# Kernel tuning notes

Hardware: AMD Instinct MI355X
Metric: run time of the kernel (lower is better)

The kernel has to match this reference:

```python
import jax, jax.numpy as jnp
import numpy as np

N = 20000      # nodes
E = 320000     # edges
H = 256        # hidden_dim
BD = 64        # bond embedding dim
MSG_IN = 2 * H + BD  # 576


def setup_inputs() -> dict:
    key = jax.random.key(0)
    ks = jax.random.split(key, 24)
    s = 0.05
    inp = {}
    inp["x"] = jax.random.randint(ks[0], (N, 3), 0, 7).astype(jnp.float32)
    inp["edge_index"] = jax.random.randint(ks[1], (2, E), 0, N).astype(jnp.int32)
    inp["edge_attr"] = jax.random.randint(ks[2], (E, 1), 0, 5).astype(jnp.float32)
    inp["batch"] = jnp.zeros((N,), jnp.int32)
    # embedding tables
    inp["atom_table"] = jax.random.normal(ks[3], (11, 64), jnp.float32) * s
    inp["charge_table"] = jax.random.normal(ks[4], (7, 32), jnp.float32) * s
    inp["hybrid_table"] = jax.random.normal(ks[5], (8, 32), jnp.float32) * s
    inp["bond_table"] = jax.random.normal(ks[6], (5, BD), jnp.float32) * s
    # 3 stacked ChemicalGraphConv layers (weights stored [in, out])
    inp["gnn_w1"] = jax.random.normal(ks[7], (3, MSG_IN, H), jnp.float32) * s
    inp["gnn_b1"] = jnp.zeros((3, H), jnp.float32)
    inp["gnn_w2"] = jax.random.normal(ks[8], (3, H, H), jnp.float32) * s
    inp["gnn_b2"] = jnp.zeros((3, H), jnp.float32)
    inp["att_w"] = jax.random.normal(ks[9], (3, BD, 1), jnp.float32) * s
    inp["att_b"] = jnp.zeros((3, 1), jnp.float32)
    # chemical_properties MLP
    inp["prop_w1"] = jax.random.normal(ks[10], (H, 128), jnp.float32) * s
    inp["prop_b1"] = jnp.zeros((128,), jnp.float32)
    inp["prop_w2"] = jax.random.normal(ks[11], (128, 32), jnp.float32) * s
    inp["prop_b2"] = jnp.zeros((32,), jnp.float32)
    # 4 functional-group pattern encoders, stacked [4, H, 16]
    inp["fg_w"] = jax.random.normal(ks[12], (4, H, 16), jnp.float32) * s
    inp["fg_b"] = jnp.zeros((4, 16), jnp.float32)
    return inp


def reference(x, edge_index, edge_attr, batch,
              atom_table, charge_table, hybrid_table, bond_table,
              gnn_w1, gnn_b1, gnn_w2, gnn_b2, att_w, att_b,
              prop_w1, prop_b1, prop_w2, prop_b2, fg_w, fg_b):
    n = x.shape[0]
    atom_types = jnp.clip(x[:, 0].astype(jnp.int32), 0, 10)
    formal_charges = jnp.clip(x[:, 2].astype(jnp.int32) + 3, 0, 6)
    hybridization = jnp.clip(x[:, 1].astype(jnp.int32), 0, 7)
    bond_types = jnp.clip(edge_attr[:, 0].astype(jnp.int32), 0, 4)
    bond_emb = bond_table[bond_types]  # [E, 64]

    h = jnp.concatenate([atom_table[atom_types],
                         charge_table[formal_charges],
                         hybrid_table[hybridization]], axis=-1)  # [N, 128]
    h = jnp.pad(h, ((0, 0), (0, H - h.shape[1])))  # pad to hidden_dim

    row, col = edge_index[0], edge_index[1]
    for l in range(3):  # 3 ChemicalGraphConv layers
        gate = jax.nn.sigmoid(bond_emb @ att_w[l] + att_b[l])            # [E, 1]
        msg = jnp.concatenate([h[row], h[col], bond_emb], axis=-1)      # [E, 576]
        msg = jax.nn.relu(msg @ gnn_w1[l] + gnn_b1[l]) @ gnn_w2[l] + gnn_b2[l]
        msg = msg * gate                                                 # [E, H]
        h = h + jax.ops.segment_sum(msg, row, num_segments=n)

    chemical_props = jax.nn.relu(h @ prop_w1 + prop_b1) @ prop_w2 + prop_b2  # [N, 32]

    # FunctionalGroupDetector: mean(encoder(h)) == mean(h) @ W + b (linear)
    pooled = jnp.mean(h, axis=0)                                   # [H]
    fg = (jnp.einsum('d,kdo->ko', pooled, fg_w) + fg_b).reshape(-1)  # [64]
    fg_features = jnp.broadcast_to(fg, (n, 64))

    return h, chemical_props, fg_features, atom_types
```

## Files before the change

kernel.cpp:

```cpp
#include <hip/hip_runtime.h>
#include <stdint.h>

typedef unsigned short u16;
typedef unsigned int   u32;
typedef __attribute__((ext_vector_type(8))) short bf16x8;
typedef __attribute__((ext_vector_type(4))) float f32x4;

#define NN 20000
#define NE 320000
#define HD 256
#define BD 64

#define WS_PRE   0u
#define WS_W1T   20480000u
#define WS_W2I   21266432u
#define WS_PW1   21659648u
#define WS_PREB  21725184u
#define WS_GATE  21740544u
#define WS_POOL  21740608u
#define WS_FGV   21741632u
#define WS_CNT   21741888u
#define WS_META  21821888u

__device__ __forceinline__ u16 f2bf(float f){
  u32 u = __float_as_uint(f);
  u += 0x7fffu + ((u >> 16) & 1u);
  return (u16)(u >> 16);
}
__device__ __forceinline__ u32 pk2(float a, float b){
  return (u32)f2bf(a) | ((u32)f2bf(b) << 16);
}
__device__ __forceinline__ float bf2f(u16 u){
  return __uint_as_float((u32)u << 16);
}
__device__ __forceinline__ u32 pk2t(float a, float b){
  return __builtin_amdgcn_perm(__float_as_uint(a), __float_as_uint(b), 0x03020706u);
}
__device__ __forceinline__ u32 relu_pack(u32 a, u32 b, float p0, float p1){
  float a0 = __uint_as_float(a << 16);
  float a1 = __uint_as_float(a & 0xffff0000u);
  float b0 = __uint_as_float(b << 16);
  float b1 = __uint_as_float(b & 0xffff0000u);
  float s0 = fmaxf(a0 + b0 + p0, 0.f);
  float s1 = fmaxf(a1 + b1 + p1, 0.f);
  return pk2t(s0, s1);
}
__device__ __forceinline__ void gl_lds16(const u16* g, u16* l){
  __builtin_amdgcn_global_load_lds(
      (const __attribute__((address_space(1))) unsigned int*)g,
      (__attribute__((address_space(3))) unsigned int*)l, 16, 0, 0);
}

__global__ void setup_k(const float* __restrict__ gw1,
                        const float* __restrict__ gw2,
                        const float* __restrict__ pw1,
                        const float* __restrict__ bond_table,
                        const float* __restrict__ gb1,
                        const float* __restrict__ att_w,
                        const float* __restrict__ att_b,
                        const float* __restrict__ x,
                        const float* __restrict__ atom_table,
                        const float* __restrict__ charge_table,
                        const float* __restrict__ hybrid_table,
                        u16* __restrict__ w1t, u16* __restrict__ w2img,
                        u16* __restrict__ pw1bf, float* __restrict__ preb,
                        float* __restrict__ gate_tab, float* __restrict__ pooled,
                        int* __restrict__ cnt,
                        float* __restrict__ h0, float* __restrict__ out_at){
  int i = blockIdx.x*256 + threadIdx.x;
  if (i < 393216){
    int l = i >> 17;
    int r = i & 131071;
    int c = r >> 8;
    int k = r & 255;
    int srow = (c < 256) ? k : (256 + k);
    w1t[i] = f2bf(gw1[(l*576 + srow)*256 + (c & 255)]);
  } else if (i < 589824){
    int t = i - 393216;
    int j  = t & 7;
    int s  = (t >> 3) & 3;
    int c  = (t >> 5) & 255;
    int ks = (t >> 13) & 7;
    int l  = t >> 16;
    int kc = s ^ ((c >> 1) & 3);
    int k  = ks*32 + kc*8 + j;
    w2img[t] = f2bf(gw2[(l*256 + k)*256 + c]);
  } else if (i < 622592){
    int t = i - 589824;
    int o = t >> 8, k = t & 255;
    pw1bf[t] = f2bf(pw1[k*128 + o]);
  } else if (i < 626432){
    int t = i - 622592;
    int l = t / 1280;
    int r = t - l*1280;
    int bt = r >> 8, c = r & 255;
    float s = gb1[l*HD + c];
    for (int d = 0; d < BD; ++d)
      s += bond_table[bt*BD + d] * gw1[(l*576 + 512 + d)*256 + c];
    preb[(l*5 + bt)*256 + c] = s;
  } else if (i < 626447){
    int t = i - 626432;
    int l = t / 5, b = t - 5*l;
    float s = att_b[l];
    for (int d = 0; d < BD; ++d) s += bond_table[b*BD + d] * att_w[l*BD + d];
    gate_tab[t] = 1.0f / (1.0f + __expf(-s));
  } else if (i < 626703){
    pooled[i - 626447] = 0.0f;
  } else if (i < 646703){
    cnt[i - 626703] = 0;
  } else if (i < 1286703){
    int t = i - 646703;
    int n = t >> 5, sub = t & 31, c0 = sub*8;
    int at = (int)x[n*3 + 0]; at = at < 0 ? 0 : (at > 10 ? 10 : at);
    float4 v0 = {0.f,0.f,0.f,0.f}, v1 = {0.f,0.f,0.f,0.f};
    if (c0 < 64){
      v0 = *(const float4*)(atom_table + at*64 + c0);
      v1 = *(const float4*)(atom_table + at*64 + c0 + 4);
    } else if (c0 < 96){
      int fc = (int)x[n*3 + 2] + 3; fc = fc < 0 ? 0 : (fc > 6 ? 6 : fc);
      v0 = *(const float4*)(charge_table + fc*32 + (c0 - 64));
      v1 = *(const float4*)(charge_table + fc*32 + (c0 - 64) + 4);
    } else if (c0 < 128){
      int hy = (int)x[n*3 + 1]; hy = hy < 0 ? 0 : (hy > 7 ? 7 : hy);
      v0 = *(const float4*)(hybrid_table + hy*32 + (c0 - 96));
      v1 = *(const float4*)(hybrid_table + hy*32 + (c0 - 96) + 4);
    }
    *(float4*)(h0 + (size_t)n*HD + c0)     = v0;
    *(float4*)(h0 + (size_t)n*HD + c0 + 4) = v1;
    if (sub == 0) out_at[n] = (float)at;
  }
}

__global__ void hist_k(const int* __restrict__ eidx, int* __restrict__ cnt){
  int e = blockIdx.x*256 + threadIdx.x;
  int r = eidx[e]; r = r < 0 ? 0 : (r >= NN ? NN-1 : r);
  atomicAdd(&cnt[r], 1);
}

__launch_bounds__(1024)
__global__ void scan_k(int* __restrict__ cnt){
  __shared__ int part[1024];
  int t = threadIdx.x;
  int base = t*20;
  int loc[20];
  int s = 0;
  #pragma unroll
  for (int j = 0; j < 20; ++j){
    int idx = base + j;
    int v = (idx < NN) ? cnt[idx] : 0;
    loc[j] = v; s += v;
  }
  part[t] = s; __syncthreads();
  for (int off = 1; off < 1024; off <<= 1){
    int v = (t >= off) ? part[t-off] : 0;
    __syncthreads();
    part[t] += v;
    __syncthreads();
  }
  int run = part[t] - s;
  #pragma unroll
  for (int j = 0; j < 20; ++j){
    int idx = base + j;
    if (idx < NN){ cnt[idx] = run; run += loc[j]; }
  }
}

__global__ void scatter_k(const int* __restrict__ eidx,
                          const float* __restrict__ eattr,
                          int* __restrict__ cur,
                          int2* __restrict__ smeta){
  int e = blockIdx.x*256 + threadIdx.x;
  int r = eidx[e];        r = r < 0 ? 0 : (r >= NN ? NN-1 : r);
  int c = eidx[NE + e];   c = c < 0 ? 0 : (c >= NN ? NN-1 : c);
  int bt = (int)eattr[e]; bt = bt < 0 ? 0 : (bt > 4 ? 4 : bt);
  int pos = atomicAdd(&cur[r], 1);
  if (pos >= 0 && pos < NE){
    int2 m; m.x = r | (bt << 20); m.y = c;
    smeta[pos] = m;
  }
}

__launch_bounds__(256, 4)
__global__ void pre_k(const float* __restrict__ h,
                      const u16* __restrict__ w1t,
                      u16* __restrict__ pre, int layer){
  __shared__ u16 a_lds[64*40];
  __shared__ u16 b_lds[256*40];
  const int tid = threadIdx.x;
  const int n0 = blockIdx.x * 64;
  const int half = blockIdx.y;
  const int w = tid >> 6, lane = tid & 63, g = lane >> 4, lr = lane & 15;
  const int rstage = tid >> 2, q = tid & 3;
  int arow = n0 + rstage; if (arow >= NN) arow = NN-1;
  const float* hrow = h + (size_t)arow*HD;
  const u16* bp = w1t + ((size_t)layer*512 + (size_t)half*256 + tid)*256;

  f32x4 acc[4][4];
  for (int mi = 0; mi < 4; ++mi)
    for (int nj = 0; nj < 4; ++nj)
      acc[mi][nj] = (f32x4){0.f,0.f,0.f,0.f};

  for (int ks = 0; ks < 8; ++ks){
    __syncthreads();
    {
      const float* src = hrow + ks*32 + q*8;
      float4 f0 = *(const float4*)src;
      float4 f1 = *(const float4*)(src + 4);
      uint4 av;
      av.x = pk2(f0.x,f0.y); av.y = pk2(f0.z,f0.w);
      av.z = pk2(f1.x,f1.y); av.w = pk2(f1.z,f1.w);
      *(uint4*)(a_lds + rstage*40 + q*8) = av;
    }
    {
      const u16* src = bp + ks*32;
      uint4 s0 = *(const uint4*)(src);
      uint4 s1 = *(const uint4*)(src + 8);
      uint4 s2 = *(const uint4*)(src + 16);
      uint4 s3 = *(const uint4*)(src + 24);
      u16* dst = b_lds + tid*40;
      *(uint4*)(dst)      = s0;
      *(uint4*)(dst + 8)  = s1;
      *(uint4*)(dst + 16) = s2;
      *(uint4*)(dst + 24) = s3;
    }
    __syncthreads();
    bf16x8 af[4], bfr[4];
    for (int mi = 0; mi < 4; ++mi)
      af[mi] = *(const bf16x8*)(a_lds + (mi*16 + lr)*40 + g*8);
    for (int nj = 0; nj < 4; ++nj)
      bfr[nj] = *(const bf16x8*)(b_lds + (w*64 + nj*16 + lr)*40 + g*8);
    for (int mi = 0; mi < 4; ++mi)
      for (int nj = 0; nj < 4; ++nj)
        acc[mi][nj] = __builtin_amdgcn_mfma_f32_16x16x32_bf16(af[mi], bfr[nj], acc[mi][nj], 0, 0, 0);
  }

  for (int mi = 0; mi < 4; ++mi)
    for (int nj = 0; nj < 4; ++nj)
      for (int p = 0; p < 4; ++p){
        int re = mi*16 + g*4 + p;
        int n = n0 + re;
        if (n < NN)
          pre[(size_t)n*512 + half*256 + w*64 + nj*16 + lr] = f2bf(acc[mi][nj][p]);
      }
}

__launch_bounds__(512, 4)
__global__ void edge_msg_k(const int2* __restrict__ smeta,
                           const u16* __restrict__ pre,
                           const float* __restrict__ prebg,
                           const u16* __restrict__ w2img,
                           const float* __restrict__ b2g,
                           const float* __restrict__ gate_tab,
                           float* __restrict__ h,
                           int layer){
  __shared__ u16 b_lds[16384];
  __shared__ u16 t_lds[64*264];
  __shared__ int   row_l[64];
  __shared__ float gate_l[64];

  const int tid = threadIdx.x;
  const int bid = blockIdx.x;
  const int blk = (bid & 7)*625 + (bid >> 3);
  const int eBase = blk * 64;
  const int w = tid >> 6, lane = tid & 63, g = lane >> 4, lr = lane & 15;
  const int rstage = tid >> 3, q = tid & 7;

  const size_t wbase = (size_t)layer*65536;

  #pragma unroll
  for (int b = 0; b < 2; ++b)
    #pragma unroll
    for (int j = 0; j < 2; ++j)
      gl_lds16(w2img + wbase + (size_t)(b*256 + w*32 + j*16)*32 + lane*8,
               b_lds + b*8192 + w*1024 + j*512);

  int2 m0 = smeta[eBase + rstage];
  const int rI  = m0.x & 0xFFFFF;
  const int btI = (m0.x >> 20) & 7;
  const int cI  = m0.y;

  if (tid < 64){
    int2 mm = smeta[eBase + tid];
    row_l[tid]  = mm.x & 0xFFFFF;
    gate_l[tid] = gate_tab[layer*5 + ((mm.x >> 20) & 7)];
  }

  {
    const u16* p1 = pre + (size_t)rI*512;
    const u16* p2 = pre + (size_t)cI*512 + 256;
    const float* pb = prebg + (size_t)(layer*5 + btI)*256;
    #pragma unroll
    for (int it = 0; it < 4; ++it){
      int c0 = it*64 + q*8;
      uint4 v1 = *(const uint4*)(p1 + c0);
      uint4 v2 = *(const uint4*)(p2 + c0);
      float4 pa = *(const float4*)(pb + c0);
      float4 pc = *(const float4*)(pb + c0 + 4);
      uint4 ov;
      ov.x = relu_pack(v1.x, v2.x, pa.x, pa.y);
      ov.y = relu_pack(v1.y, v2.y, pa.z, pa.w);
      ov.z = relu_pack(v1.z, v2.z, pc.x, pc.y);
      ov.w = relu_pack(v1.w, v2.w, pc.z, pc.w);
      *(uint4*)(t_lds + rstage*264 + c0) = ov;
    }
  }

  __syncthreads();

  f32x4 acc[4][2];
  for (int mi = 0; mi < 4; ++mi)
    for (int nj = 0; nj < 2; ++nj)
      acc[mi][nj] = (f32x4){0.f,0.f,0.f,0.f};

  const int sw = (g ^ ((lr >> 1) & 3)) << 3;

  #pragma unroll
  for (int ks = 0; ks < 8; ++ks){
    if (ks >= 1 && ks < 7){
      #pragma unroll
      for (int j = 0; j < 2; ++j)
        gl_lds16(w2img + wbase + (size_t)((ks+1)*256 + w*32 + j*16)*32 + lane*8,
                 b_lds + ((ks+1)&1)*8192 + w*1024 + j*512);
      asm volatile("s_waitcnt vmcnt(2)" ::: "memory");
    } else if (ks == 0){
      asm volatile("s_waitcnt vmcnt(2)" ::: "memory");
    } else {
      asm volatile("s_waitcnt vmcnt(0)" ::: "memory");
    }
    const u16* bb = b_lds + (ks&1)*8192 + w*1024;
    bf16x8 af[4], bfr[2];
    for (int nj = 0; nj < 2; ++nj)
      bfr[nj] = *(const bf16x8*)(bb + (nj*16 + lr)*32 + sw);
    for (int mi = 0; mi < 4; ++mi)
      af[mi] = *(const bf16x8*)(t_lds + (mi*16 + lr)*264 + ks*32 + g*8);
    __builtin_amdgcn_s_setprio(1);
    for (int mi = 0; mi < 4; ++mi)
      for (int nj = 0; nj < 2; ++nj)
        acc[mi][nj] = __builtin_amdgcn_mfma_f32_16x16x32_bf16(af[mi], bfr[nj], acc[mi][nj], 0, 0, 0);
    __builtin_amdgcn_s_setprio(0);
  }

  {
    float b2v[2];
    for (int nj = 0; nj < 2; ++nj) b2v[nj] = b2g[layer*HD + w*32 + nj*16 + lr];
    for (int mi = 0; mi < 4; ++mi)
      for (int nj = 0; nj < 2; ++nj){
        u16* mb = b_lds + nj*8192 + w*1024 + lr*64;
        float v[4];
        #pragma unroll
        for (int p = 0; p < 4; ++p){
          int re = mi*16 + g*4 + p;
          v[p] = (acc[mi][nj][p] + b2v[nj]) * gate_l[re];
        }
        int slot = (mi*2 + (g >> 1)) ^ (lr & 7);
        uint2 pkv; pkv.x = pk2t(v[0], v[1]); pkv.y = pk2t(v[2], v[3]);
        *(uint2*)(mb + slot*8 + (g & 1)*4) = pkv;
      }
  }
  __syncthreads();

  {
    const int cl = tid & 255, half = tid >> 8;
    const u16* mb = b_lds + ((cl >> 4) & 1)*8192 + (cl >> 5)*1024 + (cl & 15)*64;
    float run = 0.f;
    int currow = row_l[half*32];
    for (int e8 = half*4; e8 < half*4 + 4; ++e8){
      bf16x8 mv = *(const bf16x8*)(mb + ((e8 ^ (cl & 7)) << 3));
      #pragma unroll
      for (int j = 0; j < 8; ++j){
        int r = row_l[e8*8 + j];
        if (r != currow){
          atomicAdd(h + (size_t)currow*HD + cl, run);
          run = 0.f; currow = r;
        }
        run += bf2f((u16)mv[j]);
      }
    }
    atomicAdd(h + (size_t)currow*HD + cl, run);
  }
}

__global__ void pool_k(const float* __restrict__ h,
                       float* __restrict__ pooled){
  int c = threadIdx.x;
  int r0 = blockIdx.x * 50;
  float s = 0.f;
  for (int r = r0; r < r0 + 50; ++r)
    s += h[(size_t)r*HD + c];
  atomicAdd(&pooled[c], s);
}

__global__ void bcast_fg_k(const float* __restrict__ pooled,
                           const float* __restrict__ fg_w,
                           const float* __restrict__ fg_b,
                           float* __restrict__ out_fg){
  __shared__ float fv[64];
  int tid = threadIdx.x;
  if (tid < 64){
    int k = tid >> 4, j = tid & 15;
    float s = 0.f;
    for (int d = 0; d < HD; ++d) s += pooled[d] * fg_w[(size_t)k*HD*16 + d*16 + j];
    fv[tid] = s / (float)NN + fg_b[k*16 + j];
  }
  __syncthreads();
  int i = blockIdx.x*256 + tid;
  out_fg[i] = fv[i & 63];
}

__launch_bounds__(256, 3)
__global__ void props_mfma_k(const float* __restrict__ h,
                             const u16* __restrict__ pw1bf,
                             const float* __restrict__ pb1,
                             const float* __restrict__ pw2,
                             const float* __restrict__ pb2,
                             float* __restrict__ outp){
  __shared__ u16 a_lds[64*40];
  __shared__ u16 b2_lds[128*40];
  __shared__ u16 t2[64*136];
  __shared__ float w2s[128*32];
  const int tid = threadIdx.x;
  const int n0 = blockIdx.x*64;
  const int w = tid >> 6, lane = tid & 63, g = lane >> 4, lr = lane & 15;
  const int rstage = tid >> 2, q = tid & 3;
  int arow = n0 + rstage; if (arow >= NN) arow = NN-1;
  const float* hrow = h + (size_t)arow*HD;

  for (int j = 0; j < 4; ++j)
    *(float4*)(w2s + tid*16 + j*4) = *(const float4*)(pw2 + tid*16 + j*4);

  const int colb = tid >> 1, halfb = tid & 1;

  f32x4 acc[4][2];
  for (int mi = 0; mi < 4; ++mi)
    for (int nj = 0; nj < 2; ++nj)
      acc[mi][nj] = (f32x4){0.f,0.f,0.f,0.f};

  for (int ks = 0; ks < 8; ++ks){
    __syncthreads();
    {
      const float* src = hrow + ks*32 + q*8;
      float4 f0 = *(const float4*)src;
      float4 f1 = *(const float4*)(src + 4);
      uint4 av;
      av.x = pk2(f0.x,f0.y); av.y = pk2(f0.z,f0.w);
      av.z = pk2(f1.x,f1.y); av.w = pk2(f1.z,f1.w);
      *(uint4*)(a_lds + rstage*40 + q*8) = av;
    }
    {
      const u16* src = pw1bf + colb*256 + ks*32 + halfb*16;
      uint4 s0 = *(const uint4*)src;
      uint4 s1 = *(const uint4*)(src + 8);
      u16* dst = b2_lds + colb*40 + halfb*16;
      *(uint4*)dst = s0; *(uint4*)(dst + 8) = s1;
    }
    __syncthreads();
    bf16x8 af[4], bfr[2];
    for (int mi = 0; mi < 4; ++mi)
      af[mi] = *(const bf16x8*)(a_lds + (mi*16 + lr)*40 + g*8);
    for (int nj = 0; nj < 2; ++nj)
      bfr[nj] = *(const bf16x8*)(b2_lds + (w*32 + nj*16 + lr)*40 + g*8);
    for (int mi = 0; mi < 4; ++mi)
      for (int nj = 0; nj < 2; ++nj)
        acc[mi][nj] = __builtin_amdgcn_mfma_f32_16x16x32_bf16(af[mi], bfr[nj], acc[mi][nj], 0, 0, 0);
  }

  {
    float b1v[2];
    for (int nj = 0; nj < 2; ++nj) b1v[nj] = pb1[w*32 + nj*16 + lr];
    for (int mi = 0; mi < 4; ++mi)
      for (int nj = 0; nj < 2; ++nj){
        int colt = w*32 + nj*16 + lr;
        for (int p = 0; p < 4; ++p){
          float v = acc[mi][nj][p] + b1v[nj];
          v = v > 0.f ? v : 0.f;
          t2[(mi*16 + g*4 + p)*136 + colt] = f2bf(v);
        }
      }
  }
  __syncthreads();

  {
    int e = tid >> 2, o0 = (tid & 3)*8;
    int n = n0 + e;
    float ap[8];
    #pragma unroll
    for (int o = 0; o < 8; ++o) ap[o] = pb2[o0 + o];
    for (int d0 = 0; d0 < 16; ++d0){
      bf16x8 tv = *(const bf16x8*)(t2 + e*136 + d0*8);
      #pragma unroll
      for (int dd = 0; dd < 8; ++dd){
        float t = bf2f((u16)tv[dd]);
        const float* wr = w2s + (d0*8 + dd)*32 + o0;
        #pragma unroll
        for (int o = 0; o < 8; ++o) ap[o] += t * wr[o];
      }
    }
    if (n < NN){
      *(float4*)(outp + (size_t)n*32 + o0)     = *(float4*)(ap);
      *(float4*)(outp + (size_t)n*32 + o0 + 4) = *(float4*)(ap + 4);
    }
  }
}

extern "C" void kernel_launch(void* const* d_in, const int* in_sizes, int n_in,
                              void* d_out, int out_size, void* d_ws, size_t ws_size,
                              hipStream_t stream) {
  const float* x            = (const float*)d_in[0];
  const int*   eidx         = (const int*)  d_in[1];
  const float* eattr        = (const float*)d_in[2];
  const float* atom_table   = (const float*)d_in[4];
  const float* charge_table = (const float*)d_in[5];
  const float* hybrid_table = (const float*)d_in[6];
  const float* bond_table   = (const float*)d_in[7];
  const float* gw1          = (const float*)d_in[8];
  const float* gb1          = (const float*)d_in[9];
  const float* gw2          = (const float*)d_in[10];
  const float* gb2          = (const float*)d_in[11];
  const float* attw         = (const float*)d_in[12];
  const float* attb         = (const float*)d_in[13];
  const float* pw1          = (const float*)d_in[14];
  const float* pb1          = (const float*)d_in[15];
  const float* pw2          = (const float*)d_in[16];
  const float* pb2          = (const float*)d_in[17];
  const float* fgw          = (const float*)d_in[18];
  const float* fgb          = (const float*)d_in[19];

  float* out       = (float*)d_out;
  float* out_h     = out;
  float* out_props = out + (size_t)NN*HD;
  float* out_fg    = out_props + (size_t)NN*32;
  float* out_at    = out_fg + (size_t)NN*64;

  char* ws = (char*)d_ws;
  u16*   pre      = (u16*)  (ws + WS_PRE);
  u16*   w1t      = (u16*)  (ws + WS_W1T);
  u16*   w2img    = (u16*)  (ws + WS_W2I);
  u16*   pw1bf    = (u16*)  (ws + WS_PW1);
  float* prebg    = (float*)(ws + WS_PREB);
  float* gate_tab = (float*)(ws + WS_GATE);
  float* pooled   = (float*)(ws + WS_POOL);
  int*   cnt      = (int*)  (ws + WS_CNT);
  int2*  smeta    = (int2*) (ws + WS_META);

  setup_k<<<5027, 256, 0, stream>>>(gw1, gw2, pw1, bond_table, gb1, attw, attb,
                                    x, atom_table, charge_table, hybrid_table,
                                    w1t, w2img, pw1bf, prebg, gate_tab, pooled,
                                    cnt, out_h, out_at);

  hist_k<<<1250, 256, 0, stream>>>(eidx, cnt);
  scan_k<<<1, 1024, 0, stream>>>(cnt);
  scatter_k<<<1250, 256, 0, stream>>>(eidx, eattr, cnt, smeta);

  for (int l = 0; l < 3; ++l){
    pre_k<<<dim3(313, 2), 256, 0, stream>>>(out_h, w1t, pre, l);
    edge_msg_k<<<5000, 512, 0, stream>>>(smeta, pre, prebg, w2img,
                                         gb2, gate_tab, out_h, l);
  }

  pool_k<<<400, 256, 0, stream>>>(out_h, pooled);
  props_mfma_k<<<313, 256, 0, stream>>>(out_h, pw1bf, pb1, pw2, pb2, out_props);
  bcast_fg_k<<<5000, 256, 0, stream>>>(pooled, fgw, fgb, out_fg);
}
```

Before: 418.6 us.

## Coalesce weight conversion reads, precompute row-boundary mask, split fg compute

Weight-conversion setup now iterates over the source arrays so global reads are coalesced and writes are scattered, which also grows the grid. In edge_msg_k, row-change boundaries are computed once per block with a wavefront ballot into a 64-bit mask, so the segmented reduction checks bits instead of reading row_l for every edge. The gather loads are batched ahead of the relu/pack math to give more loads in flight. The functional-group matvec moves into its own single-block kernel so the 5000 broadcast blocks no longer each repeat the 256-long dot products.

New measurement: 382.9 us. -8.5%, faster.

```diff
diff --git a/kernel.cpp b/kernel.cpp
--- a/kernel.cpp
+++ b/kernel.cpp
@@ -3,6 +3,7 @@
 
 typedef unsigned short u16;
 typedef unsigned int   u32;
+typedef unsigned long long u64;
 typedef __attribute__((ext_vector_type(8))) short bf16x8;
 typedef __attribute__((ext_vector_type(4))) float f32x4;
 
@@ -68,29 +69,32 @@
                         int* __restrict__ cnt,
                         float* __restrict__ h0, float* __restrict__ out_at){
   int i = blockIdx.x*256 + threadIdx.x;
-  if (i < 393216){
-    int l = i >> 17;
-    int r = i & 131071;
-    int c = r >> 8;
-    int k = r & 255;
-    int srow = (c < 256) ? k : (256 + k);
-    w1t[i] = f2bf(gw1[(l*576 + srow)*256 + (c & 255)]);
-  } else if (i < 589824){
-    int t = i - 393216;
-    int j  = t & 7;
-    int s  = (t >> 3) & 3;
-    int c  = (t >> 5) & 255;
-    int ks = (t >> 13) & 7;
-    int l  = t >> 16;
-    int kc = s ^ ((c >> 1) & 3);
-    int k  = ks*32 + kc*8 + j;
-    w2img[t] = f2bf(gw2[(l*256 + k)*256 + c]);
-  } else if (i < 622592){
-    int t = i - 589824;
-    int o = t >> 8, k = t & 255;
-    pw1bf[t] = f2bf(pw1[k*128 + o]);
-  } else if (i < 626432){
-    int t = i - 622592;
+  if (i < 442368){
+    float v = gw1[i];
+    int l = i / 147456;
+    int r = i - l*147456;
+    int srow = r >> 8, c = r & 255;
+    if (srow < 512){
+      int dc = (srow < 256) ? c : (256 + c);
+      w1t[((size_t)l*512 + dc)*256 + (srow & 255)] = f2bf(v);
+    }
+  } else if (i < 638976){
+    int t = i - 442368;
+    float v = gw2[t];
+    int l = t >> 16;
+    int rest = t & 65535;
+    int k = rest >> 8, c = rest & 255;
+    int ks = k >> 5, k5 = k & 31;
+    int kc = k5 >> 3, j = k5 & 7;
+    int s = kc ^ ((c >> 1) & 3);
+    w2img[(((l*8 + ks)*256 + c)*4 + s)*8 + j] = f2bf(v);
+  } else if (i < 671744){
+    int t = i - 638976;
+    float v = pw1[t];
+    int k = t >> 7, o = t & 127;
+    pw1bf[o*256 + k] = f2bf(v);
+  } else if (i < 675584){
+    int t = i - 671744;
     int l = t / 1280;
     int r = t - l*1280;
     int bt = r >> 8, c = r & 255;
@@ -98,18 +102,18 @@
     for (int d = 0; d < BD; ++d)
       s += bond_table[bt*BD + d] * gw1[(l*576 + 512 + d)*256 + c];
     preb[(l*5 + bt)*256 + c] = s;
-  } else if (i < 626447){
-    int t = i - 626432;
+  } else if (i < 675599){
+    int t = i - 675584;
     int l = t / 5, b = t - 5*l;
     float s = att_b[l];
     for (int d = 0; d < BD; ++d) s += bond_table[b*BD + d] * att_w[l*BD + d];
     gate_tab[t] = 1.0f / (1.0f + __expf(-s));
-  } else if (i < 626703){
-    pooled[i - 626447] = 0.0f;
-  } else if (i < 646703){
-    cnt[i - 626703] = 0;
-  } else if (i < 1286703){
-    int t = i - 646703;
+  } else if (i < 675855){
+    pooled[i - 675599] = 0.0f;
+  } else if (i < 695855){
+    cnt[i - 675855] = 0;
+  } else if (i < 1335855){
+    int t = i - 695855;
     int n = t >> 5, sub = t & 31, c0 = sub*8;
     int at = (int)x[n*3 + 0]; at = at < 0 ? 0 : (at > 10 ? 10 : at);
     float4 v0 = {0.f,0.f,0.f,0.f}, v1 = {0.f,0.f,0.f,0.f};
@@ -257,6 +261,7 @@
   __shared__ u16 t_lds[64*264];
   __shared__ int   row_l[64];
   __shared__ float gate_l[64];
+  __shared__ u64   mask_l;
 
   const int tid = threadIdx.x;
   const int bid = blockIdx.x;
@@ -281,26 +286,36 @@
 
   if (tid < 64){
     int2 mm = smeta[eBase + tid];
-    row_l[tid]  = mm.x & 0xFFFFF;
+    int r = mm.x & 0xFFFFF;
+    row_l[tid]  = r;
     gate_l[tid] = gate_tab[layer*5 + ((mm.x >> 20) & 7)];
+    int rprev = __shfl_up(r, 1);
+    bool fl = (tid > 0) && (r != rprev);
+    u64 mk = __ballot(fl);
+    if (tid == 0) mask_l = mk;
   }
 
   {
     const u16* p1 = pre + (size_t)rI*512;
     const u16* p2 = pre + (size_t)cI*512 + 256;
     const float* pb = prebg + (size_t)(layer*5 + btI)*256;
+    uint4 v1[4], v2[4];
     #pragma unroll
     for (int it = 0; it < 4; ++it){
       int c0 = it*64 + q*8;
-      uint4 v1 = *(const uint4*)(p1 + c0);
-      uint4 v2 = *(const uint4*)(p2 + c0);
+      v1[it] = *(const uint4*)(p1 + c0);
+      v2[it] = *(const uint4*)(p2 + c0);
+    }
+    #pragma unroll
+    for (int it = 0; it < 4; ++it){
+      int c0 = it*64 + q*8;
       float4 pa = *(const float4*)(pb + c0);
       float4 pc = *(const float4*)(pb + c0 + 4);
       uint4 ov;
-      ov.x = relu_pack(v1.x, v2.x, pa.x, pa.y);
-      ov.y = relu_pack(v1.y, v2.y, pa.z, pa.w);
-      ov.z = relu_pack(v1.z, v2.z, pc.x, pc.y);
-      ov.w = relu_pack(v1.w, v2.w, pc.z, pc.w);
+      ov.x = relu_pack(v1[it].x, v2[it].x, pa.x, pa.y);
+      ov.y = relu_pack(v1[it].y, v2[it].y, pa.z, pa.w);
+      ov.z = relu_pack(v1[it].z, v2[it].z, pc.x, pc.y);
+      ov.w = relu_pack(v1[it].w, v2[it].w, pc.z, pc.w);
       *(uint4*)(t_lds + rstage*264 + c0) = ov;
     }
   }
@@ -361,22 +376,27 @@
 
   {
     const int cl = tid & 255, half = tid >> 8;
+    u64 mk = mask_l;
+    u32 m32 = (u32)(mk >> (half ? 32 : 0));
+    m32 = __builtin_amdgcn_readfirstlane(m32);
     const u16* mb = b_lds + ((cl >> 4) & 1)*8192 + (cl >> 5)*1024 + (cl & 15)*64;
     float run = 0.f;
-    int currow = row_l[half*32];
-    for (int e8 = half*4; e8 < half*4 + 4; ++e8){
+    #pragma unroll
+    for (int e8l = 0; e8l < 4; ++e8l){
+      int e8 = half*4 + e8l;
       bf16x8 mv = *(const bf16x8*)(mb + ((e8 ^ (cl & 7)) << 3));
       #pragma unroll
       for (int j = 0; j < 8; ++j){
-        int r = row_l[e8*8 + j];
-        if (r != currow){
-          atomicAdd(h + (size_t)currow*HD + cl, run);
-          run = 0.f; currow = r;
+        int el = e8l*8 + j;
+        run += bf2f((u16)mv[j]);
+        bool fl = (el == 31) || ((m32 >> (el + 1)) & 1u);
+        if (fl){
+          int rr = row_l[half*32 + el];
+          atomicAdd(h + (size_t)rr*HD + cl, run);
+          run = 0.f;
         }
-        run += bf2f((u16)mv[j]);
       }
     }
-    atomicAdd(h + (size_t)currow*HD + cl, run);
   }
 }
 
@@ -390,20 +410,23 @@
   atomicAdd(&pooled[c], s);
 }
 
-__global__ void bcast_fg_k(const float* __restrict__ pooled,
-                           const float* __restrict__ fg_w,
-                           const float* __restrict__ fg_b,
+__global__ void fg_k(const float* __restrict__ pooled,
+                     const float* __restrict__ fg_w,
+                     const float* __restrict__ fg_b,
+                     float* __restrict__ fg_vals){
+  int o = threadIdx.x;
+  int k = o >> 4, j = o & 15;
+  float s = 0.f;
+  for (int d = 0; d < HD; ++d) s += pooled[d] * fg_w[(size_t)k*HD*16 + d*16 + j];
+  fg_vals[o] = s / (float)NN + fg_b[k*16 + j];
+}
+
+__global__ void bcast_fg_k(const float* __restrict__ fg_vals,
                            float* __restrict__ out_fg){
   __shared__ float fv[64];
-  int tid = threadIdx.x;
-  if (tid < 64){
-    int k = tid >> 4, j = tid & 15;
-    float s = 0.f;
-    for (int d = 0; d < HD; ++d) s += pooled[d] * fg_w[(size_t)k*HD*16 + d*16 + j];
-    fv[tid] = s / (float)NN + fg_b[k*16 + j];
-  }
+  if (threadIdx.x < 64) fv[threadIdx.x] = fg_vals[threadIdx.x];
   __syncthreads();
-  int i = blockIdx.x*256 + tid;
+  int i = blockIdx.x*256 + threadIdx.x;
   out_fg[i] = fv[i & 63];
 }
 
@@ -539,10 +562,11 @@
   float* prebg    = (float*)(ws + WS_PREB);
   float* gate_tab = (float*)(ws + WS_GATE);
   float* pooled   = (float*)(ws + WS_POOL);
+  float* fg_vals  = (float*)(ws + WS_FGV);
   int*   cnt      = (int*)  (ws + WS_CNT);
   int2*  smeta    = (int2*) (ws + WS_META);
 
-  setup_k<<<5027, 256, 0, stream>>>(gw1, gw2, pw1, bond_table, gb1, attw, attb,
+  setup_k<<<5219, 256, 0, stream>>>(gw1, gw2, pw1, bond_table, gb1, attw, attb,
                                     x, atom_table, charge_table, hybrid_table,
                                     w1t, w2img, pw1bf, prebg, gate_tab, pooled,
                                     cnt, out_h, out_at);
@@ -558,6 +582,7 @@
   }
 
   pool_k<<<400, 256, 0, stream>>>(out_h, pooled);
+  fg_k<<<1, 64, 0, stream>>>(pooled, fgw, fgb, fg_vals);
   props_mfma_k<<<313, 256, 0, stream>>>(out_h, pw1bf, pb1, pw2, pb2, out_props);
-  bcast_fg_k<<<5000, 256, 0, stream>>>(pooled, fgw, fgb, out_fg);
-}
+  bcast_fg_k<<<5000, 256, 0, stream>>>(fg_vals, out_fg);
+}
```
